# Optimization experiments

Hardware: AMD Instinct MI355X
Metric: run time of the kernel (lower is better)

Reference implementation:

```python
import jax, jax.numpy as jnp
import numpy as np

NUM_HEADS = 16
HIDDEN = 1024
TOTAL = 2048
NSEG = 8


def setup_inputs() -> dict:
    key = jax.random.key(0)
    ks = jax.random.split(key, 10)
    x = jax.random.normal(ks[0], (TOTAL, HIDDEN), dtype=jnp.float32)
    # cu_seqlens: [0, b1, ..., TOTAL], sorted segment boundaries
    inner = np.sort(np.random.default_rng(0).integers(1, TOTAL, size=NSEG - 1))
    cu_seqlens = jnp.asarray(np.concatenate([[0], inner, [TOTAL]]), dtype=jnp.int32)
    s = 1.0 / np.sqrt(HIDDEN)
    def lin(k):
        kw, kb = jax.random.split(k)
        W = jax.random.uniform(kw, (HIDDEN, HIDDEN), jnp.float32, -s, s)
        b = jax.random.uniform(kb, (HIDDEN,), jnp.float32, -s, s)
        return W, b
    Wq, bq = lin(ks[1]); Wk, bk = lin(ks[2]); Wv, bv = lin(ks[3]); Wo, bo = lin(ks[4])
    return {"hidden_states_packed": x, "cu_seqlens": cu_seqlens,
            "Wq": Wq, "bq": bq, "Wk": Wk, "bk": bk,
            "Wv": Wv, "bv": bv, "Wo": Wo, "bo": bo}


def reference(hidden_states_packed, cu_seqlens, Wq, bq, Wk, bk, Wv, bv, Wo, bo):
    T, H = hidden_states_packed.shape
    dh = H // NUM_HEADS
    x = hidden_states_packed
    q = (x @ Wq.T + bq).reshape(T, NUM_HEADS, dh)
    k = (x @ Wk.T + bk).reshape(T, NUM_HEADS, dh)
    v = (x @ Wv.T + bv).reshape(T, NUM_HEADS, dh)
    # segment id of each token from cu_seqlens boundaries
    seg = jnp.searchsorted(cu_seqlens, jnp.arange(T, dtype=jnp.int32), side="right")
    same_seg = seg[:, None] == seg[None, :]  # [T, T] block-diagonal mask
    scale = 1.0 / jnp.sqrt(jnp.asarray(dh, x.dtype))
    scores = jnp.einsum("qhd,khd->hqk", q, k) * scale  # [H, T, T]
    neg = jnp.asarray(jnp.finfo(scores.dtype).min, scores.dtype)
    scores = jnp.where(same_seg[None, :, :], scores, neg)
    attn = jax.nn.softmax(scores, axis=-1)
    ctx = jnp.einsum("hqk,khd->qhd", attn, v).reshape(T, H)
    return ctx @ Wo.T + bo
```

## Files before the change

### kernel.cpp

```cpp
#include <hip/hip_runtime.h>

typedef _Float16 f16x8 __attribute__((ext_vector_type(8)));
typedef _Float16 f16x4 __attribute__((ext_vector_type(4)));
typedef float    f32x4 __attribute__((ext_vector_type(4)));

#define MFMA_F16(a, b, c) __builtin_amdgcn_mfma_f32_16x16x32_f16((a), (b), (c), 0, 0, 0)

typedef __attribute__((address_space(1))) void gas_void;
typedef __attribute__((address_space(3))) void las_void;
#define GLOAD_LDS16(g, l) \
  __builtin_amdgcn_global_load_lds((gas_void*)(g), (las_void*)(l), 16, 0, 0)

#define NEG_INF (-__builtin_inff())

constexpr int T_SEQ  = 2048;
constexpr int HID    = 1024;
constexpr int NHEADS = 16;
constexpr int DH     = 64;
constexpr int NSEG   = 8;

__global__ __launch_bounds__(256) void convert_all(
    const float* __restrict__ x,
    const float* __restrict__ Wq, const float* __restrict__ Wk,
    const float* __restrict__ Wv, const float* __restrict__ Wo,
    _Float16* __restrict__ xh,
    _Float16* __restrict__ Wqh, _Float16* __restrict__ Wkh,
    _Float16* __restrict__ Wvh, _Float16* __restrict__ Woh) {
  int i = blockIdx.x * 256 + threadIdx.x;
  const float* src;
  _Float16* dst;
  int local;
  if (i < 524288) {
    src = x; dst = xh; local = i;
  } else {
    int j = i - 524288;
    int w = j >> 18;
    local = j & 262143;
    src = (w == 0) ? Wq : (w == 1) ? Wk : (w == 2) ? Wv : Wo;
    dst = (w == 0) ? Wqh : (w == 1) ? Wkh : (w == 2) ? Wvh : Woh;
  }
  float4 f = *(const float4*)(src + (size_t)local * 4);
  f16x4 h;
  h[0] = (_Float16)f.x; h[1] = (_Float16)f.y;
  h[2] = (_Float16)f.z; h[3] = (_Float16)f.w;
  *(f16x4*)(dst + (size_t)local * 4) = h;
}

template <int LAYOUT, int BM, int BN>
__device__ __forceinline__ void gemm_t(const _Float16* __restrict__ A,
                                       const _Float16* __restrict__ B,
                                       const float* __restrict__ bias,
                                       _Float16* __restrict__ outh,
                                       float* __restrict__ outf) {
  constexpr int K = HID, N = HID;
  constexpr int MI = BM / 32;
  constexpr int NI = BN / 32;
  constexpr int LA = (BM * 64) / (256 * 8);
  constexpr int LB = (BN * 64) / (256 * 8);
  __shared__ _Float16 As[BM * 64];
  __shared__ _Float16 Bs[BN * 64];
  const int tid  = threadIdx.x;
  const int wave = tid >> 6, lane = tid & 63;
  const int lr = lane & 15, lq = lane >> 4;
  const int wm = (wave >> 1) * (BM / 2);
  const int wn = (wave & 1) * (BN / 2);
  const int bm = blockIdx.y * BM, bn = blockIdx.x * BN;

  const _Float16* gA[LA];
  const _Float16* gB[LB];
  _Float16* lA[LA];
  _Float16* lB[LB];
#pragma unroll
  for (int i = 0; i < LA; ++i) {
    const int s = i * 256 + tid;
    const int row = s >> 3, pch = s & 7;
    const int lch = pch ^ (row & 7);
    gA[i] = A + (size_t)(bm + row) * K + lch * 8;
    lA[i] = &As[(i * 256 + wave * 64) * 8];
  }
#pragma unroll
  for (int i = 0; i < LB; ++i) {
    const int s = i * 256 + tid;
    const int row = s >> 3, pch = s & 7;
    const int lch = pch ^ (row & 7);
    gB[i] = B + (size_t)(bn + row) * K + lch * 8;
    lB[i] = &Bs[(i * 256 + wave * 64) * 8];
  }

  f32x4 acc[MI][NI] = {};

  for (int kk = 0; kk < K; kk += 64) {
#pragma unroll
    for (int i = 0; i < LA; ++i) GLOAD_LDS16(gA[i] + kk, lA[i]);
#pragma unroll
    for (int i = 0; i < LB; ++i) GLOAD_LDS16(gB[i] + kk, lB[i]);
    __syncthreads();
#pragma unroll
    for (int ks = 0; ks < 2; ++ks) {
      f16x8 af[MI], bf[NI];
#pragma unroll
      for (int mi = 0; mi < MI; ++mi) {
        const int row = wm + mi * 16 + lr;
        af[mi] = *(const f16x8*)&As[row * 64 + (((ks * 4 + lq) ^ (row & 7)) * 8)];
      }
#pragma unroll
      for (int ni = 0; ni < NI; ++ni) {
        const int row = wn + ni * 16 + lr;
        bf[ni] = *(const f16x8*)&Bs[row * 64 + (((ks * 4 + lq) ^ (row & 7)) * 8)];
      }
#pragma unroll
      for (int mi = 0; mi < MI; ++mi)
#pragma unroll
        for (int ni = 0; ni < NI; ++ni)
          acc[mi][ni] = MFMA_F16(af[mi], bf[ni], acc[mi][ni]);
    }
    __syncthreads();
  }

#pragma unroll
  for (int ni = 0; ni < NI; ++ni) {
    const int col = bn + wn + ni * 16 + lr;
    const float bv = bias[col];
#pragma unroll
    for (int mi = 0; mi < MI; ++mi) {
      const f32x4 v = acc[mi][ni];
      const int row0 = bm + wm + mi * 16 + lq * 4;
      if (LAYOUT == 3) {
        f16x4 o;
#pragma unroll
        for (int r = 0; r < 4; ++r) o[r] = (_Float16)(v[r] + bv);
        *(f16x4*)&outh[(size_t)col * T_SEQ + row0] = o;
      } else {
#pragma unroll
        for (int r = 0; r < 4; ++r) {
          const int row = row0 + r;
          const float val = v[r] + bv;
          if (LAYOUT == 0)
            outh[((size_t)(col >> 6) * T_SEQ + row) * DH + (col & 63)] = (_Float16)val;
          else
            outf[(size_t)row * N + col] = val;
        }
      }
    }
  }
}

__global__ __launch_bounds__(256) void gemm_qkv(
    const _Float16* __restrict__ xh,
    const _Float16* __restrict__ Wqh, const _Float16* __restrict__ Wkh,
    const _Float16* __restrict__ Wvh,
    const float* __restrict__ bq, const float* __restrict__ bk,
    const float* __restrict__ bv,
    _Float16* __restrict__ qp, _Float16* __restrict__ kp,
    _Float16* __restrict__ vT) {
  const int z = blockIdx.z;
  if (z == 0) {
    gemm_t<0, 64, 128>(xh, Wqh, bq, qp, nullptr);
  } else if (z == 1) {
    gemm_t<0, 64, 128>(xh, Wkh, bk, kp, nullptr);
  } else {
    gemm_t<3, 64, 128>(xh, Wvh, bv, vT, nullptr);
  }
}

__global__ __launch_bounds__(256) void gemm_out(
    const _Float16* __restrict__ ctxh, const _Float16* __restrict__ Woh,
    const float* __restrict__ bo, float* __restrict__ out) {
  gemm_t<1, 64, 64>(ctxh, Woh, bo, nullptr, out);
}

__device__ __forceinline__ float redsum16(float v) {
  v += __shfl_xor(v, 1);
  v += __shfl_xor(v, 2);
  v += __shfl_xor(v, 4);
  v += __shfl_xor(v, 8);
  return v;
}

__global__ __launch_bounds__(512, 4) void attn_kernel(
    const _Float16* __restrict__ qp, const _Float16* __restrict__ kp,
    const _Float16* __restrict__ vT, const int* __restrict__ cu,
    _Float16* __restrict__ ctx) {
  constexpr float SCL2E = 0.125f * 1.44269504f;
  constexpr int PSTR = 72;
  __shared__ _Float16 Ks[2][64 * 64];
  __shared__ _Float16 Vs[2][64 * 64];
  __shared__ _Float16 Pl[8][16 * PSTR];
  float* mO = (float*)&Ks[0][0];
  float* mL = (float*)&Vs[0][0];
  const int bx   = blockIdx.x;
  const int xcd  = bx & 7;
  const int idx  = bx >> 3;
  const int hsel = idx & 1;
  const int h    = xcd + 8 * hsel;
  const int q0   = ((((idx >> 1) + hsel * 16) & 31)) * 64;
  const int tid = threadIdx.x, wave = tid >> 6, lane = tid & 63;
  const int lr = lane & 15, lq = lane >> 4;
  const int qsub = wave & 3, khalf = wave >> 2;
  const int qw = q0 + qsub * 16;

  int cs[NSEG + 1];
#pragma unroll
  for (int i = 0; i <= NSEG; ++i) cs[i] = cu[i];

  int sstart[4], send[4];
#pragma unroll
  for (int r = 0; r < 4; ++r) {
    const int row = qw + lq * 4 + r;
    sstart[r] = 0; send[r] = T_SEQ;
#pragma unroll
    for (int s = 0; s < NSEG; ++s)
      if (row >= cs[s] && row < cs[s + 1]) { sstart[r] = cs[s]; send[r] = cs[s + 1]; }
  }
  int wlo = 0, whi = T_SEQ, wlo2 = 0;
#pragma unroll
  for (int s = 0; s < NSEG; ++s) {
    if (qw >= cs[s] && qw < cs[s + 1]) { wlo = cs[s]; whi = cs[s + 1]; }
    if (qw + 15 >= cs[s] && qw + 15 < cs[s + 1]) wlo2 = cs[s];
  }
  const bool wsame = (wlo == wlo2);
  int klo = 0, khi = T_SEQ;
#pragma unroll
  for (int s = 0; s < NSEG; ++s) {
    if (q0 >= cs[s] && q0 < cs[s + 1]) klo = cs[s];
    if (q0 + 63 >= cs[s] && q0 + 63 < cs[s + 1]) khi = cs[s + 1];
  }
  klo &= ~63;
  const int range  = khi - klo;
  const int hlen   = ((range + 127) >> 7) << 6;
  const int nsteps = hlen >> 6;
  const int kstart = klo + khalf * hlen;

  const _Float16* qbase = qp + ((size_t)h * T_SEQ + qw + lr) * DH;
  f16x8 qf0 = *(const f16x8*)(qbase + lq * 8);
  f16x8 qf1 = *(const f16x8*)(qbase + 32 + lq * 8);
#pragma unroll
  for (int i = 0; i < 8; ++i) {
    qf0[i] = qf0[i] * (_Float16)SCL2E;
    qf1[i] = qf1[i] * (_Float16)SCL2E;
  }

  const _Float16* kb = kp + (size_t)h * T_SEQ * DH;
  const _Float16* vb = vT + (size_t)h * DH * T_SEQ;

  const int ht = qsub * 64 + lane;
  int kRow[2], kCol[2], vRow[2], vCol[2];
  _Float16* lK[2];
  _Float16* lV[2];
#pragma unroll
  for (int i = 0; i < 2; ++i) {
    const int s = i * 256 + ht;
    const int row = s >> 3, pch = s & 7;
    const int lch = pch ^ (row & 7);
    kRow[i] = row; kCol[i] = lch * 8;
    vRow[i] = row; vCol[i] = lch * 8;
    lK[i] = &Ks[khalf][(i * 256 + qsub * 64) * 8];
    lV[i] = &Vs[khalf][(i * 256 + qsub * 64) * 8];
  }

  float lst[4] = {0.f, 0.f, 0.f, 0.f};
  f32x4 oacc[4];
#pragma unroll
  for (int c = 0; c < 4; ++c) oacc[c] = f32x4{0.f, 0.f, 0.f, 0.f};

  _Float16* pw = &Pl[wave][0];

  for (int s = 0; s < nsteps; ++s) {
    const int kt = kstart + s * 64;
#pragma unroll
    for (int i = 0; i < 2; ++i) {
      const int grow = min(kt + kRow[i], T_SEQ - 1);
      GLOAD_LDS16(kb + (size_t)grow * DH + kCol[i], lK[i]);
    }
#pragma unroll
    for (int i = 0; i < 2; ++i) {
      const int gcol = min(kt + vCol[i], T_SEQ - 8);
      GLOAD_LDS16(vb + (size_t)vRow[i] * T_SEQ + gcol, lV[i]);
    }
    __syncthreads();

    f32x4 sc[4];
#pragma unroll
    for (int n = 0; n < 4; ++n) {
      const int row = n * 16 + lr;
      const f16x8 kf0 =
          *(const f16x8*)&Ks[khalf][row * 64 + (((0 * 4 + lq) ^ (row & 7)) * 8)];
      const f16x8 kf1 =
          *(const f16x8*)&Ks[khalf][row * 64 + (((1 * 4 + lq) ^ (row & 7)) * 8)];
      sc[n] = f32x4{0.f, 0.f, 0.f, 0.f};
      sc[n] = MFMA_F16(qf0, kf0, sc[n]);
      sc[n] = MFMA_F16(qf1, kf1, sc[n]);
    }
    const bool fastTile = wsame && (kt >= wlo) && (kt + 64 <= whi);
    if (fastTile) {
#pragma unroll
      for (int r = 0; r < 4; ++r) {
        float p[4];
#pragma unroll
        for (int n = 0; n < 4; ++n) p[n] = exp2f(sc[n][r]);
        lst[r] += (p[0] + p[1]) + (p[2] + p[3]);
        _Float16* pr = &pw[(lq * 4 + r) * PSTR + lr];
        pr[0]  = (_Float16)p[0];
        pr[16] = (_Float16)p[1];
        pr[32] = (_Float16)p[2];
        pr[48] = (_Float16)p[3];
      }
    } else {
#pragma unroll
      for (int r = 0; r < 4; ++r) {
        float p[4];
#pragma unroll
        for (int n = 0; n < 4; ++n) {
          const int col = kt + n * 16 + lr;
          const float vv =
              (col >= sstart[r] && col < send[r]) ? sc[n][r] : NEG_INF;
          p[n] = exp2f(vv);
        }
        lst[r] += (p[0] + p[1]) + (p[2] + p[3]);
        _Float16* pr = &pw[(lq * 4 + r) * PSTR + lr];
        pr[0]  = (_Float16)p[0];
        pr[16] = (_Float16)p[1];
        pr[32] = (_Float16)p[2];
        pr[48] = (_Float16)p[3];
      }
    }
    const f16x8 pf0 = *(const f16x8*)&pw[lr * PSTR + lq * 8];
    const f16x8 pf1 = *(const f16x8*)&pw[lr * PSTR + 32 + lq * 8];
#pragma unroll
    for (int c = 0; c < 4; ++c) {
      const int row = c * 16 + lr;
      const f16x8 vf0 =
          *(const f16x8*)&Vs[khalf][row * 64 + (((0 * 4 + lq) ^ (row & 7)) * 8)];
      const f16x8 vf1 =
          *(const f16x8*)&Vs[khalf][row * 64 + (((1 * 4 + lq) ^ (row & 7)) * 8)];
      oacc[c] = MFMA_F16(pf0, vf0, oacc[c]);
      oacc[c] = MFMA_F16(pf1, vf1, oacc[c]);
    }
    __syncthreads();
  }

#pragma unroll
  for (int r = 0; r < 4; ++r) lst[r] = redsum16(lst[r]);

  if (khalf) {
#pragma unroll
    for (int c = 0; c < 4; ++c)
#pragma unroll
      for (int r = 0; r < 4; ++r)
        mO[((qsub * 16) + lq * 4 + r) * 64 + c * 16 + lr] = oacc[c][r];
    if (lr == 0) {
#pragma unroll
      for (int r = 0; r < 4; ++r) mL[qsub * 16 + lq * 4 + r] = lst[r];
    }
  }
  __syncthreads();
  if (!khalf) {
#pragma unroll
    for (int r = 0; r < 4; ++r) lst[r] += mL[qsub * 16 + lq * 4 + r];
#pragma unroll
    for (int c = 0; c < 4; ++c)
#pragma unroll
      for (int r = 0; r < 4; ++r) {
        const int row = qw + lq * 4 + r;
        const float val =
            (oacc[c][r] + mO[((qsub * 16) + lq * 4 + r) * 64 + c * 16 + lr]) /
            lst[r];
        ctx[(size_t)row * HID + h * DH + c * 16 + lr] = (_Float16)val;
      }
  }
}

extern "C" void kernel_launch(void* const* d_in, const int* in_sizes, int n_in,
                              void* d_out, int out_size, void* d_ws, size_t ws_size,
                              hipStream_t stream) {
  const float* x  = (const float*)d_in[0];
  const int* cu   = (const int*)d_in[1];
  const float* Wq = (const float*)d_in[2]; const float* bq = (const float*)d_in[3];
  const float* Wk = (const float*)d_in[4]; const float* bk = (const float*)d_in[5];
  const float* Wv = (const float*)d_in[6]; const float* bv = (const float*)d_in[7];
  const float* Wo = (const float*)d_in[8]; const float* bo = (const float*)d_in[9];
  float* out = (float*)d_out;

  char* ws = (char*)d_ws;
  _Float16* xh   = (_Float16*)(ws + (size_t)0);
  _Float16* Wqh  = (_Float16*)(ws + ((size_t)4 << 20));
  _Float16* Wkh  = (_Float16*)(ws + ((size_t)6 << 20));
  _Float16* Wvh  = (_Float16*)(ws + ((size_t)8 << 20));
  _Float16* Woh  = (_Float16*)(ws + ((size_t)10 << 20));
  _Float16* qp   = (_Float16*)(ws + ((size_t)12 << 20));
  _Float16* kp   = (_Float16*)(ws + ((size_t)16 << 20));
  _Float16* vT   = (_Float16*)(ws + ((size_t)20 << 20));
  _Float16* ctxh = (_Float16*)(ws + ((size_t)24 << 20));

  convert_all<<<6144, 256, 0, stream>>>(x, Wq, Wk, Wv, Wo, xh, Wqh, Wkh, Wvh, Woh);
  gemm_qkv<<<dim3(8, 32, 3), 256, 0, stream>>>(xh, Wqh, Wkh, Wvh, bq, bk, bv, qp, kp, vT);
  attn_kernel<<<512, 512, 0, stream>>>(qp, kp, vT, cu, ctxh);
  gemm_out<<<dim3(16, 32), 256, 0, stream>>>(ctxh, Woh, bo, out);
}
```

Baseline: 135.0 us.

## Load K/V fragments directly from global and give each wave its own key range

Drops the shared-memory staging of K and V tiles and their per-step block barriers. Each wave now reads its MFMA operands straight from global memory (relying on L1/L2) and iterates only over key tiles spanning its own 16-row query window, split between two halves, instead of the whole 64-row block's range. This trims masked work and synchronisation, but four waves per key half now fetch the same K/V data redundantly through cache, and the global reads are less coalesced.

```diff
diff --git a/kernel.cpp b/kernel.cpp
--- a/kernel.cpp
+++ b/kernel.cpp
@@ -183,11 +183,9 @@
     _Float16* __restrict__ ctx) {
   constexpr float SCL2E = 0.125f * 1.44269504f;
   constexpr int PSTR = 72;
-  __shared__ _Float16 Ks[2][64 * 64];
-  __shared__ _Float16 Vs[2][64 * 64];
   __shared__ _Float16 Pl[8][16 * PSTR];
-  float* mO = (float*)&Ks[0][0];
-  float* mL = (float*)&Vs[0][0];
+  __shared__ float mO[4][16][64];
+  __shared__ float mL[4][16];
   const int bx   = blockIdx.x;
   const int xcd  = bx & 7;
   const int idx  = bx >> 3;
@@ -212,24 +210,28 @@
     for (int s = 0; s < NSEG; ++s)
       if (row >= cs[s] && row < cs[s + 1]) { sstart[r] = cs[s]; send[r] = cs[s + 1]; }
   }
-  int wlo = 0, whi = T_SEQ, wlo2 = 0;
+  int wlo = 0, whi = T_SEQ, wlo2 = 0, whi2 = T_SEQ;
 #pragma unroll
   for (int s = 0; s < NSEG; ++s) {
     if (qw >= cs[s] && qw < cs[s + 1]) { wlo = cs[s]; whi = cs[s + 1]; }
-    if (qw + 15 >= cs[s] && qw + 15 < cs[s + 1]) wlo2 = cs[s];
+    if (qw + 15 >= cs[s] && qw + 15 < cs[s + 1]) { wlo2 = cs[s]; whi2 = cs[s + 1]; }
   }
   const bool wsame = (wlo == wlo2);
-  int klo = 0, khi = T_SEQ;
-#pragma unroll
-  for (int s = 0; s < NSEG; ++s) {
-    if (q0 >= cs[s] && q0 < cs[s + 1]) klo = cs[s];
-    if (q0 + 63 >= cs[s] && q0 + 63 < cs[s + 1]) khi = cs[s + 1];
-  }
-  klo &= ~63;
-  const int range  = khi - klo;
-  const int hlen   = ((range + 127) >> 7) << 6;
-  const int nsteps = hlen >> 6;
-  const int kstart = klo + khalf * hlen;
+  const int a = wlo, b = whi2;
+  const int t0    = a & ~63;
+  const int ntile = (b - t0 + 63) >> 6;
+  const int nt0   = (ntile + 1) >> 1;
+  const int tiles = khalf ? (ntile - nt0) : nt0;
+  const int tstart = khalf ? (t0 + nt0 * 64) : t0;
+  const int mid   = t0 + nt0 * 64;
+  const int st    = khalf ? mid : a;
+  const int en    = khalf ? b : (mid < b ? mid : b);
+  int vlo[4], vhi[4];
+#pragma unroll
+  for (int r = 0; r < 4; ++r) {
+    vlo[r] = sstart[r] > st ? sstart[r] : st;
+    vhi[r] = send[r] < en ? send[r] : en;
+  }
 
   const _Float16* qbase = qp + ((size_t)h * T_SEQ + qw + lr) * DH;
   f16x8 qf0 = *(const f16x8*)(qbase + lq * 8);
@@ -243,21 +245,6 @@
   const _Float16* kb = kp + (size_t)h * T_SEQ * DH;
   const _Float16* vb = vT + (size_t)h * DH * T_SEQ;
 
-  const int ht = qsub * 64 + lane;
-  int kRow[2], kCol[2], vRow[2], vCol[2];
-  _Float16* lK[2];
-  _Float16* lV[2];
-#pragma unroll
-  for (int i = 0; i < 2; ++i) {
-    const int s = i * 256 + ht;
-    const int row = s >> 3, pch = s & 7;
-    const int lch = pch ^ (row & 7);
-    kRow[i] = row; kCol[i] = lch * 8;
-    vRow[i] = row; vCol[i] = lch * 8;
-    lK[i] = &Ks[khalf][(i * 256 + qsub * 64) * 8];
-    lV[i] = &Vs[khalf][(i * 256 + qsub * 64) * 8];
-  }
-
   float lst[4] = {0.f, 0.f, 0.f, 0.f};
   f32x4 oacc[4];
 #pragma unroll
@@ -265,33 +252,19 @@
 
   _Float16* pw = &Pl[wave][0];
 
-  for (int s = 0; s < nsteps; ++s) {
-    const int kt = kstart + s * 64;
-#pragma unroll
-    for (int i = 0; i < 2; ++i) {
-      const int grow = min(kt + kRow[i], T_SEQ - 1);
-      GLOAD_LDS16(kb + (size_t)grow * DH + kCol[i], lK[i]);
-    }
-#pragma unroll
-    for (int i = 0; i < 2; ++i) {
-      const int gcol = min(kt + vCol[i], T_SEQ - 8);
-      GLOAD_LDS16(vb + (size_t)vRow[i] * T_SEQ + gcol, lV[i]);
-    }
-    __syncthreads();
-
+  for (int s = 0; s < tiles; ++s) {
+    const int kt = tstart + s * 64;
     f32x4 sc[4];
 #pragma unroll
     for (int n = 0; n < 4; ++n) {
-      const int row = n * 16 + lr;
-      const f16x8 kf0 =
-          *(const f16x8*)&Ks[khalf][row * 64 + (((0 * 4 + lq) ^ (row & 7)) * 8)];
-      const f16x8 kf1 =
-          *(const f16x8*)&Ks[khalf][row * 64 + (((1 * 4 + lq) ^ (row & 7)) * 8)];
+      const _Float16* kr = kb + (size_t)(kt + n * 16 + lr) * DH + lq * 8;
+      const f16x8 kf0 = *(const f16x8*)kr;
+      const f16x8 kf1 = *(const f16x8*)(kr + 32);
       sc[n] = f32x4{0.f, 0.f, 0.f, 0.f};
       sc[n] = MFMA_F16(qf0, kf0, sc[n]);
       sc[n] = MFMA_F16(qf1, kf1, sc[n]);
     }
-    const bool fastTile = wsame && (kt >= wlo) && (kt + 64 <= whi);
+    const bool fastTile = wsame && (kt >= st) && (kt + 64 <= en);
     if (fastTile) {
 #pragma unroll
       for (int r = 0; r < 4; ++r) {
@@ -313,7 +286,7 @@
         for (int n = 0; n < 4; ++n) {
           const int col = kt + n * 16 + lr;
           const float vv =
-              (col >= sstart[r] && col < send[r]) ? sc[n][r] : NEG_INF;
+              (col >= vlo[r] && col < vhi[r]) ? sc[n][r] : NEG_INF;
           p[n] = exp2f(vv);
         }
         lst[r] += (p[0] + p[1]) + (p[2] + p[3]);
@@ -328,15 +301,12 @@
     const f16x8 pf1 = *(const f16x8*)&pw[lr * PSTR + 32 + lq * 8];
 #pragma unroll
     for (int c = 0; c < 4; ++c) {
-      const int row = c * 16 + lr;
-      const f16x8 vf0 =
-          *(const f16x8*)&Vs[khalf][row * 64 + (((0 * 4 + lq) ^ (row & 7)) * 8)];
-      const f16x8 vf1 =
-          *(const f16x8*)&Vs[khalf][row * 64 + (((1 * 4 + lq) ^ (row & 7)) * 8)];
+      const _Float16* vr = vb + (size_t)(c * 16 + lr) * T_SEQ + kt + lq * 8;
+      const f16x8 vf0 = *(const f16x8*)vr;
+      const f16x8 vf1 = *(const f16x8*)(vr + 32);
       oacc[c] = MFMA_F16(pf0, vf0, oacc[c]);
       oacc[c] = MFMA_F16(pf1, vf1, oacc[c]);
     }
-    __syncthreads();
   }
 
 #pragma unroll
@@ -347,24 +317,23 @@
     for (int c = 0; c < 4; ++c)
 #pragma unroll
       for (int r = 0; r < 4; ++r)
-        mO[((qsub * 16) + lq * 4 + r) * 64 + c * 16 + lr] = oacc[c][r];
+        mO[qsub][lq * 4 + r][c * 16 + lr] = oacc[c][r];
     if (lr == 0) {
 #pragma unroll
-      for (int r = 0; r < 4; ++r) mL[qsub * 16 + lq * 4 + r] = lst[r];
+      for (int r = 0; r < 4; ++r) mL[qsub][lq * 4 + r] = lst[r];
     }
   }
   __syncthreads();
   if (!khalf) {
 #pragma unroll
-    for (int r = 0; r < 4; ++r) lst[r] += mL[qsub * 16 + lq * 4 + r];
+    for (int r = 0; r < 4; ++r) lst[r] += mL[qsub][lq * 4 + r];
 #pragma unroll
     for (int c = 0; c < 4; ++c)
 #pragma unroll
       for (int r = 0; r < 4; ++r) {
         const int row = qw + lq * 4 + r;
         const float val =
-            (oacc[c][r] + mO[((qsub * 16) + lq * 4 + r) * 64 + c * 16 + lr]) /
-            lst[r];
+            (oacc[c][r] + mO[qsub][lq * 4 + r][c * 16 + lr]) / lst[r];
         ctx[(size_t)row * HID + h * DH + c * 16 + lr] = (_Float16)val;
       }
   }
```

After: 150.0 us. 11.1% more time.

## Double-buffer LDS tiles in GEMM to overlap global loads with MFMA

Applied to the files above, without the earlier changes.

The GEMM main loop now uses two LDS buffers for the A and B tiles. It issues the async global-to-LDS loads for the next K-tile before computing on the current one, and halves the number of barriers per tile. This is meant to hide global memory latency behind the matrix-core work. In exchange the GEMM doubles its shared memory use, which can lower occupancy.

```diff
diff --git a/kernel.cpp b/kernel.cpp
--- a/kernel.cpp
+++ b/kernel.cpp
@@ -53,12 +53,15 @@
                                        _Float16* __restrict__ outh,
                                        float* __restrict__ outf) {
   constexpr int K = HID, N = HID;
+  constexpr int NT = K / 64;
   constexpr int MI = BM / 32;
   constexpr int NI = BN / 32;
   constexpr int LA = (BM * 64) / (256 * 8);
   constexpr int LB = (BN * 64) / (256 * 8);
-  __shared__ _Float16 As[BM * 64];
-  __shared__ _Float16 Bs[BN * 64];
+  __shared__ _Float16 As0[BM * 64];
+  __shared__ _Float16 As1[BM * 64];
+  __shared__ _Float16 Bs0[BN * 64];
+  __shared__ _Float16 Bs1[BN * 64];
   const int tid  = threadIdx.x;
   const int wave = tid >> 6, lane = tid & 63;
   const int lr = lane & 15, lq = lane >> 4;
@@ -68,15 +71,14 @@
 
   const _Float16* gA[LA];
   const _Float16* gB[LB];
-  _Float16* lA[LA];
-  _Float16* lB[LB];
+  int oA[LA], oB[LB];
 #pragma unroll
   for (int i = 0; i < LA; ++i) {
     const int s = i * 256 + tid;
     const int row = s >> 3, pch = s & 7;
     const int lch = pch ^ (row & 7);
     gA[i] = A + (size_t)(bm + row) * K + lch * 8;
-    lA[i] = &As[(i * 256 + wave * 64) * 8];
+    oA[i] = (i * 256 + wave * 64) * 8;
   }
 #pragma unroll
   for (int i = 0; i < LB; ++i) {
@@ -84,29 +86,30 @@
     const int row = s >> 3, pch = s & 7;
     const int lch = pch ^ (row & 7);
     gB[i] = B + (size_t)(bn + row) * K + lch * 8;
-    lB[i] = &Bs[(i * 256 + wave * 64) * 8];
+    oB[i] = (i * 256 + wave * 64) * 8;
   }
 
   f32x4 acc[MI][NI] = {};
 
-  for (int kk = 0; kk < K; kk += 64) {
-#pragma unroll
-    for (int i = 0; i < LA; ++i) GLOAD_LDS16(gA[i] + kk, lA[i]);
-#pragma unroll
-    for (int i = 0; i < LB; ++i) GLOAD_LDS16(gB[i] + kk, lB[i]);
-    __syncthreads();
+  auto stage = [&](_Float16 (&as)[BM * 64], _Float16 (&bs)[BN * 64], int kk) {
+#pragma unroll
+    for (int i = 0; i < LA; ++i) GLOAD_LDS16(gA[i] + kk, &as[oA[i]]);
+#pragma unroll
+    for (int i = 0; i < LB; ++i) GLOAD_LDS16(gB[i] + kk, &bs[oB[i]]);
+  };
+  auto compute = [&](_Float16 (&as)[BM * 64], _Float16 (&bs)[BN * 64]) {
 #pragma unroll
     for (int ks = 0; ks < 2; ++ks) {
       f16x8 af[MI], bf[NI];
 #pragma unroll
       for (int mi = 0; mi < MI; ++mi) {
         const int row = wm + mi * 16 + lr;
-        af[mi] = *(const f16x8*)&As[row * 64 + (((ks * 4 + lq) ^ (row & 7)) * 8)];
+        af[mi] = *(const f16x8*)&as[row * 64 + (((ks * 4 + lq) ^ (row & 7)) * 8)];
       }
 #pragma unroll
       for (int ni = 0; ni < NI; ++ni) {
         const int row = wn + ni * 16 + lr;
-        bf[ni] = *(const f16x8*)&Bs[row * 64 + (((ks * 4 + lq) ^ (row & 7)) * 8)];
+        bf[ni] = *(const f16x8*)&bs[row * 64 + (((ks * 4 + lq) ^ (row & 7)) * 8)];
       }
 #pragma unroll
       for (int mi = 0; mi < MI; ++mi)
@@ -114,6 +117,16 @@
         for (int ni = 0; ni < NI; ++ni)
           acc[mi][ni] = MFMA_F16(af[mi], bf[ni], acc[mi][ni]);
     }
+  };
+
+  stage(As0, Bs0, 0);
+  __syncthreads();
+  for (int t = 0; t < NT; t += 2) {
+    stage(As1, Bs1, (t + 1) * 64);
+    compute(As0, Bs0);
+    __syncthreads();
+    if (t + 2 < NT) stage(As0, Bs0, (t + 2) * 64);
+    compute(As1, Bs1);
     __syncthreads();
   }
 
```

Result: slower. 153.5 us (+13.7%).
